# Kernel tuning notes

Measured on AMD Instinct MI355X. Metric: run time of the kernel, lower is better.

The kernel has to match this reference:

```python
import jax, jax.numpy as jnp
import numpy as np

B, S, D, H = 8, 1024, 1024, 16
HD = D // H  # head_dim = 64
MAX_LEN = 1024


def setup_inputs() -> dict:
    key = jax.random.key(0)
    k1, k2, k3, k4, k5 = jax.random.split(key, 5)
    return {
        "query": jax.random.normal(k1, (B, S, D), dtype=jnp.float32),
        "key": jax.random.normal(k2, (B, S, D), dtype=jnp.float32),
        "value": jax.random.normal(k3, (B, S, D), dtype=jnp.float32),
        "rel_pos_k": jax.random.normal(k4, (MAX_LEN, HD), dtype=jnp.float32) * 0.02,
        "rel_pos_v": jax.random.normal(k5, (MAX_LEN, HD), dtype=jnp.float32) * 0.02,
    }


def _circular_indices(seq_len):
    i = jnp.arange(seq_len)
    d = (i[:, None] - i[None, :] + seq_len) % seq_len  # (S, S)
    return jnp.minimum(d, seq_len - d)


def reference(query, key, value, rel_pos_k, rel_pos_v):
    b, s, dm = query.shape
    hd = dm // H
    # (b, h, s, hd)
    q = query.reshape(b, s, H, hd).transpose(0, 2, 1, 3)
    k = key.reshape(b, s, H, hd).transpose(0, 2, 1, 3)
    v = value.reshape(b, s, H, hd).transpose(0, 2, 1, 3)

    scale = 1.0 / np.sqrt(hd)
    scores = jnp.einsum('bhqd,bhkd->bhqk', q, k) * scale

    idx = _circular_indices(s)                 # (s, s) int
    rel_k = rel_pos_k[idx]                     # (s, s, hd)
    rel_v = rel_pos_v[idx]                     # (s, s, hd)

    scores = scores + jnp.einsum('bhqd,qkd->bhqk', q, rel_k)
    attn_weights = jax.nn.softmax(scores, axis=-1)

    out = jnp.einsum('bhqk,bhkd->bhqd', attn_weights, v)
    out = out + jnp.einsum('bhqk,qkd->bhqd', attn_weights, rel_v)

    return out.transpose(0, 2, 1, 3).reshape(b, s, dm)
```

## Files before the change

### kernel.cpp

```cpp
#include <hip/hip_runtime.h>

typedef _Float16 f16;
typedef __attribute__((ext_vector_type(4))) _Float16 f16x4;
typedef __attribute__((ext_vector_type(8))) _Float16 f16x8;
typedef __attribute__((ext_vector_type(4))) float f32x4;
typedef __attribute__((ext_vector_type(4))) unsigned int u32x4;

#define BB 8
#define SS 1024
#define DD 1024
#define HH 16
#define HD 64
#define QPB 32
#define PROW 1040
#define TSTR 520
#define KSTR 72
#define RVSTR 520

#define VT_ELEMS  ((size_t)BB * HH * HD * SS)
#define RVT_ELEMS ((size_t)HD * RVSTR)
#define RKT_ELEMS ((size_t)513 * HD)
#define KT_ELEMS  ((size_t)BB * HH * SS * HD)
#define WS_PART ((VT_ELEMS + RVT_ELEMS + RKT_ELEMS) * 2)
#define WS_FULL ((VT_ELEMS + RVT_ELEMS + RKT_ELEMS + KT_ELEMS) * 2)

__device__ inline f16x8 cvt16(float4 a, float4 b) {
  f16x8 h;
  h[0] = (f16)a.x; h[1] = (f16)a.y; h[2] = (f16)a.z; h[3] = (f16)a.w;
  h[4] = (f16)b.x; h[5] = (f16)b.y; h[6] = (f16)b.z; h[7] = (f16)b.w;
  return h;
}

__device__ inline f16x8 funnel8(u32x4 lo, u32x4 hi, int sh, unsigned lob) {
  unsigned e0 = (sh & 1) ? lo.y : lo.x;
  unsigned e1 = (sh & 1) ? lo.z : lo.y;
  unsigned e2 = (sh & 1) ? lo.w : lo.z;
  unsigned e3 = (sh & 1) ? hi.x : lo.w;
  unsigned e4 = (sh & 1) ? hi.y : hi.x;
  unsigned f0 = (sh & 2) ? e2 : e0;
  unsigned f1 = (sh & 2) ? e3 : e1;
  unsigned f2 = (sh & 2) ? e4 : e2;
  unsigned f3 = (sh & 2) ? ((sh & 1) ? hi.z : hi.y) : e3;
  unsigned f4 = (sh & 2) ? ((sh & 1) ? hi.w : hi.z) : e4;
  union { u32x4 u; f16x8 h; } o;
  o.u.x = __builtin_amdgcn_alignbit(f1, f0, lob);
  o.u.y = __builtin_amdgcn_alignbit(f2, f1, lob);
  o.u.z = __builtin_amdgcn_alignbit(f3, f2, lob);
  o.u.w = __builtin_amdgcn_alignbit(f4, f3, lob);
  return o.h;
}

__device__ inline f16x8 rev8(f16x8 v) {
  union { u32x4 u; f16x8 h; } i, o;
  i.h = v;
  o.u.x = __builtin_amdgcn_alignbit(i.u.w, i.u.w, 16);
  o.u.y = __builtin_amdgcn_alignbit(i.u.z, i.u.z, 16);
  o.u.z = __builtin_amdgcn_alignbit(i.u.y, i.u.y, 16);
  o.u.w = __builtin_amdgcn_alignbit(i.u.x, i.u.x, 16);
  return o.h;
}

__global__ __launch_bounds__(256, 2)
void prep_kernel(const float* __restrict__ Vg, const float* __restrict__ Rvg,
                 const float* __restrict__ Kg, const float* __restrict__ Rkg,
                 f16* __restrict__ Vt, f16* __restrict__ Rvt,
                 f16* __restrict__ Rkt, f16* __restrict__ Kt) {
  __shared__ __align__(16) f16 Tt[64 * KSTR];
  const int tid = threadIdx.x;
  const int bid = blockIdx.x;

  if (bid < 2056) {
    const int sr = tid >> 2, cs = (tid & 3) * 16;
    const float* src;
    int srcstride;
    f16* dst;
    int dststride, dstcol;
    if (bid < 2048) {
      int b = bid >> 8, h = (bid >> 4) & 15, tc = bid & 15;
      src = Vg + ((size_t)(b * SS + tc * 64)) * DD + h * HD;
      srcstride = DD;
      dst = Vt + ((size_t)((b * HH + h) * HD)) * SS;
      dststride = SS; dstcol = tc * 64;
    } else {
      int cc = bid - 2048;
      src = Rvg + ((size_t)(cc * 64)) * HD;
      srcstride = HD;
      dst = Rvt;
      dststride = RVSTR; dstcol = cc * 64;
    }
    {
      const float* s = src + (size_t)sr * srcstride + cs;
      float4 v0 = *(const float4*)(s);
      float4 v1 = *(const float4*)(s + 4);
      float4 v2 = *(const float4*)(s + 8);
      float4 v3 = *(const float4*)(s + 12);
      *(f16x8*)(Tt + sr * KSTR + cs) = cvt16(v0, v1);
      *(f16x8*)(Tt + sr * KSTR + cs + 8) = cvt16(v2, v3);
    }
    __syncthreads();
    {
      f16x8 o0, o1;
      #pragma unroll
      for (int i = 0; i < 8; ++i) o0[i] = Tt[(cs + i) * KSTR + sr];
      #pragma unroll
      for (int i = 0; i < 8; ++i) o1[i] = Tt[(cs + 8 + i) * KSTR + sr];
      f16* o = dst + (size_t)sr * dststride + dstcol + cs;
      *(f16x8*)(o) = o0;
      *(f16x8*)(o + 8) = o1;
    }
  } else if (bid < 2058) {
    const int base = (bid - 2056) * 16416;
    for (int j = tid; j < 16416; j += 256)
      Rkt[base + j] = (f16)Rkg[base + j];
  } else {
    const int n = bid - 2058;
    #pragma unroll
    for (int jj = 0; jj < 4; ++jj) {
      int o4 = n * 1024 + jj * 256 + tid;
      int d4 = o4 & 15;
      int s  = (o4 >> 4) & 1023;
      int bh = o4 >> 14;
      int b = bh >> 4, h = bh & 15;
      float4 v = *(const float4*)(Kg + ((size_t)(b * SS + s)) * DD + h * HD + d4 * 4);
      f16x4 hv; hv[0] = (f16)v.x; hv[1] = (f16)v.y; hv[2] = (f16)v.z; hv[3] = (f16)v.w;
      *(f16x4*)(Kt + (size_t)o4 * 4) = hv;
    }
  }
}

template <bool KT16>
__global__ __launch_bounds__(1024, 4)
void circ_attn_v11(const float* __restrict__ Qg, const float* __restrict__ Kg,
                   const f16* __restrict__ Kt, const f16* __restrict__ Rkt,
                   const float* __restrict__ Rkg, const float* __restrict__ Rvg,
                   const f16* __restrict__ Vt, const f16* __restrict__ Rvt,
                   float* __restrict__ Out) {
  __shared__ __align__(16) f16 Pf[QPB * PROW];
  __shared__ __align__(16) f16 Tb[QPB * TSTR];
  __shared__ __align__(16) f16 Qls[QPB * KSTR];
  __shared__ float lsw[16][32];
  __shared__ float w512[32];

  const int i = blockIdx.x;
  const int g = ((i >> 8) << 3) | (i & 7);
  const int m = (i >> 3) & 31;
  const int b = g >> 4;
  const int h = g & 15;
  const int q0 = m * QPB;

  const int tid = threadIdx.x;
  const int w = tid >> 6;
  const int lane = tid & 63;
  const int quad = lane >> 4;
  const int l16 = lane & 15;
  const int wd = w & 3;
  const int wh = w >> 2;

  if (tid < 256) {
    const int r = tid >> 3;
    const int cg = tid & 7;
    const float* qsrc = Qg + ((size_t)(b * SS + q0 + r)) * DD + h * HD + cg * 8;
    float4 u0 = *(const float4*)(qsrc);
    float4 u1 = *(const float4*)(qsrc + 4);
    *(f16x8*)(Qls + r * KSTR + cg * 8) = cvt16(u0, u1);
  }
  __syncthreads();

  f16x8 qa0, qa1, qb0, qb1;
  {
    const f16* qp = Qls + l16 * KSTR + quad * 8;
    qa0 = *(const f16x8*)(qp);
    qa1 = *(const f16x8*)(qp + 32);
    const f16* qp2 = Qls + (16 + l16) * KSTR + quad * 8;
    qb0 = *(const f16x8*)(qp2);
    qb1 = *(const f16x8*)(qp2 + 32);
  }

  {
    const f16* rkp = Rkt + ((size_t)(w * 16 + l16)) * HD + quad * 8;
    f16x8 t0[2], t1[2];
    #pragma unroll
    for (int t = 0; t < 2; ++t) {
      const f16* np = rkp + (size_t)t * 256 * HD;
      t0[t] = *(const f16x8*)(np);
      t1[t] = *(const f16x8*)(np + 32);
    }
    #pragma unroll
    for (int cc = 0; cc < 2; ++cc) {
      f32x4 ca = {0.f, 0.f, 0.f, 0.f};
      ca = __builtin_amdgcn_mfma_f32_16x16x32_f16(qa0, t0[cc], ca, 0, 0, 0);
      ca = __builtin_amdgcn_mfma_f32_16x16x32_f16(qa1, t1[cc], ca, 0, 0, 0);
      f32x4 cb = {0.f, 0.f, 0.f, 0.f};
      cb = __builtin_amdgcn_mfma_f32_16x16x32_f16(qb0, t0[cc], cb, 0, 0, 0);
      cb = __builtin_amdgcn_mfma_f32_16x16x32_f16(qb1, t1[cc], cb, 0, 0, 0);
      const int dbase = cc * 256 + w * 16 + l16;
      #pragma unroll
      for (int r = 0; r < 4; ++r) {
        Tb[(quad * 4 + r) * TSTR + dbase] = (f16)ca[r];
        Tb[(16 + quad * 4 + r) * TSTR + dbase] = (f16)cb[r];
      }
    }
  }
  if (w == 0) {
    const float* rk = Rkg + 512 * HD;
    float ta = 0.f, tb = 0.f;
    #pragma unroll
    for (int j = 0; j < 8; ++j) {
      float rkv0 = rk[quad * 8 + j], rkv1 = rk[32 + quad * 8 + j];
      ta += (float)qa0[j] * rkv0 + (float)qa1[j] * rkv1;
      tb += (float)qb0[j] * rkv0 + (float)qb1[j] * rkv1;
    }
    ta += __shfl_xor(ta, 16); ta += __shfl_xor(ta, 32);
    tb += __shfl_xor(tb, 16); tb += __shfl_xor(tb, 32);
    if (quad == 0) {
      Tb[l16 * TSTR + 512] = (f16)ta;
      Tb[(16 + l16) * TSTR + 512] = (f16)tb;
    }
  }

  const f16* kp16 = KT16 ?
      (Kt + (((size_t)(b * HH + h) << 10) + w * 16 + l16) * HD + quad * 8) : nullptr;
  const float* kp32 = KT16 ? nullptr :
      (Kg + ((size_t)(b * SS + w * 16 + l16)) * DD + h * HD + quad * 8);
  f16x8 k0[4], k1[4];
  float4 f0, f1, f2, f3;
  if (KT16) {
    #pragma unroll
    for (int t = 0; t < 4; ++t) {
      const f16* np = kp16 + (size_t)t * 256 * HD;
      k0[t] = *(const f16x8*)(np);
      k1[t] = *(const f16x8*)(np + 32);
    }
  } else {
    f0 = *(const float4*)(kp32);
    f1 = *(const float4*)(kp32 + 4);
    f2 = *(const float4*)(kp32 + 32);
    f3 = *(const float4*)(kp32 + 36);
  }
  __syncthreads();

  {
    float psa = 0.f, psb = 0.f;
    #pragma unroll
    for (int kc = 0; kc < 4; ++kc) {
      f16x8 c0, c1;
      if (KT16) {
        c0 = k0[kc]; c1 = k1[kc];
      } else {
        c0 = cvt16(f0, f1); c1 = cvt16(f2, f3);
        if (kc < 3) {
          const float* s = kp32 + (size_t)(kc + 1) * 256 * DD;
          f0 = *(const float4*)(s);      f1 = *(const float4*)(s + 4);
          f2 = *(const float4*)(s + 32); f3 = *(const float4*)(s + 36);
        }
      }
      const int kb_ = kc * 256 + w * 16 + quad * 4;
      const int j0a = ((q0 + l16) - kb_) & 1023;
      const int j0b = (j0a + 16) & 1023;
      float tva[4], tvb[4];
      #pragma unroll
      for (int r = 0; r < 4; ++r) {
        int jra = (j0a - r) & 1023;
        int da = (jra < 1024 - jra) ? jra : 1024 - jra;
        tva[r] = (float)Tb[l16 * TSTR + da];
        int jrb = (j0b - r) & 1023;
        int db = (jrb < 1024 - jrb) ? jrb : 1024 - jrb;
        tvb[r] = (float)Tb[(16 + l16) * TSTR + db];
      }
      f32x4 ca = {0.f, 0.f, 0.f, 0.f};
      ca = __builtin_amdgcn_mfma_f32_16x16x32_f16(c0, qa0, ca, 0, 0, 0);
      ca = __builtin_amdgcn_mfma_f32_16x16x32_f16(c1, qa1, ca, 0, 0, 0);
      f32x4 cb = {0.f, 0.f, 0.f, 0.f};
      cb = __builtin_amdgcn_mfma_f32_16x16x32_f16(c0, qb0, cb, 0, 0, 0);
      cb = __builtin_amdgcn_mfma_f32_16x16x32_f16(c1, qb1, cb, 0, 0, 0);
      f16x4 pva, pvb;
      #pragma unroll
      for (int r = 0; r < 4; ++r) {
        float sa = fmaf(ca[r], 0.125f, tva[r]);
        float pa = __expf(sa);
        pva[r] = (f16)pa; psa += pa;
        float sb = fmaf(cb[r], 0.125f, tvb[r]);
        float pb = __expf(sb);
        pvb[r] = (f16)pb; psb += pb;
      }
      *(f16x4*)(Pf + l16 * PROW + kb_) = pva;
      *(f16x4*)(Pf + (16 + l16) * PROW + kb_) = pvb;
    }
    psa += __shfl_xor(psa, 16); psa += __shfl_xor(psa, 32);
    psb += __shfl_xor(psb, 16); psb += __shfl_xor(psb, 32);
    if (quad == 0) {
      lsw[w][l16] = psa;
      lsw[w][16 + l16] = psb;
    }
  }
  if (w == 0 && lane < 32)
    *(f16x8*)(Pf + lane * PROW + 1024) = *(const f16x8*)(Pf + lane * PROW);

  const f16* vtp = Vt + ((size_t)((b * HH + h) * HD) + wd * 16 + l16) * SS
                      + wh * 256 + quad * 8;
  f16x8 v0[4], v1[4];
  #pragma unroll
  for (int t = 0; t < 4; ++t) {
    v0[t] = *(const f16x8*)(vtp + t * 64);
    v1[t] = *(const f16x8*)(vtp + t * 64 + 32);
  }
  __syncthreads();

  f32x4 coa = {0.f, 0.f, 0.f, 0.f};
  f32x4 cob = {0.f, 0.f, 0.f, 0.f};
  {
    #pragma unroll
    for (int kc = 0; kc < 4; ++kc) {
      const int jb = wh * 256 + kc * 64 + quad * 8;
      f16x8 ap0 = *(const f16x8*)(Pf + l16 * PROW + jb);
      f16x8 ap1 = *(const f16x8*)(Pf + l16 * PROW + jb + 32);
      coa = __builtin_amdgcn_mfma_f32_16x16x32_f16(ap0, v0[kc], coa, 0, 0, 0);
      coa = __builtin_amdgcn_mfma_f32_16x16x32_f16(ap1, v1[kc], coa, 0, 0, 0);
      f16x8 bp0 = *(const f16x8*)(Pf + (16 + l16) * PROW + jb);
      f16x8 bp1 = *(const f16x8*)(Pf + (16 + l16) * PROW + jb + 32);
      cob = __builtin_amdgcn_mfma_f32_16x16x32_f16(bp0, v0[kc], cob, 0, 0, 0);
      cob = __builtin_amdgcn_mfma_f32_16x16x32_f16(bp1, v1[kc], cob, 0, 0, 0);
    }
  }

  const f16* rvp = Rvt + ((size_t)(wd * 16 + l16)) * RVSTR + wh * 128 + quad * 8;
  f16x8 r0[2], r1[2];
  #pragma unroll
  for (int t = 0; t < 2; ++t) {
    r0[t] = *(const f16x8*)(rvp + t * 64);
    r1[t] = *(const f16x8*)(rvp + t * 64 + 32);
  }

  #pragma unroll
  for (int it = 0; it < 2; ++it) {
    const int flat = it * 1024 + tid;
    const int ql = flat >> 6;
    const int gg = flat & 63;
    const int qq = q0 + ql;
    const f16* rowp = Pf + ql * PROW;
    const int sp = qq & 7;
    const int bp = (qq + 8 * gg) & 1023;
    const f16* app = rowp + (bp - sp);
    u32x4 pA = *(const u32x4*)(app);
    u32x4 pB = *(const u32x4*)(app + 8);
    const int sm = (qq + 1) & 7;
    const int bm = (qq - 8 * gg - 7) & 1023;
    const f16* apm = rowp + (bm - sm);
    u32x4 mA = *(const u32x4*)(apm);
    u32x4 mB = *(const u32x4*)(apm + 8);
    f16x8 pp = funnel8(pA, pB, sp >> 1, (unsigned)((sp & 1) * 16));
    f16x8 mw = funnel8(mA, mB, sm >> 1, (unsigned)((sm & 1) * 16));
    f16x8 rm = rev8(mw);
    f16x8 wv = rm + pp;
    if (gg == 0) wv[0] = rm[0];
    *(f16x8*)(Tb + ql * TSTR + gg * 8) = wv;
  }
  if (tid < 32)
    w512[tid] = (float)Pf[tid * PROW + ((q0 + tid + 512) & 1023)];
  __syncthreads();

  {
    #pragma unroll
    for (int cc = 0; cc < 2; ++cc) {
      const int jb = wh * 128 + cc * 64 + quad * 8;
      f16x8 aw0 = *(const f16x8*)(Tb + l16 * TSTR + jb);
      f16x8 aw1 = *(const f16x8*)(Tb + l16 * TSTR + jb + 32);
      coa = __builtin_amdgcn_mfma_f32_16x16x32_f16(aw0, r0[cc], coa, 0, 0, 0);
      coa = __builtin_amdgcn_mfma_f32_16x16x32_f16(aw1, r1[cc], coa, 0, 0, 0);
      f16x8 bw0 = *(const f16x8*)(Tb + (16 + l16) * TSTR + jb);
      f16x8 bw1 = *(const f16x8*)(Tb + (16 + l16) * TSTR + jb + 32);
      cob = __builtin_amdgcn_mfma_f32_16x16x32_f16(bw0, r0[cc], cob, 0, 0, 0);
      cob = __builtin_amdgcn_mfma_f32_16x16x32_f16(bw1, r1[cc], cob, 0, 0, 0);
    }
  }

  if (wh > 0) {
    float* st = (float*)Pf + ((size_t)(((wh - 1) * 4 + wd) * 64 + lane)) * 8;
    *(f32x4*)(st) = coa;
    *(f32x4*)(st + 4) = cob;
  }
  __syncthreads();
  if (wh == 0) {
    #pragma unroll
    for (int p = 0; p < 3; ++p) {
      const float* st = (const float*)Pf + ((size_t)((p * 4 + wd) * 64 + lane)) * 8;
      coa += *(const f32x4*)(st);
      cob += *(const f32x4*)(st + 4);
    }
    const int d = wd * 16 + l16;
    const float rv512 = Rvg[512 * HD + d];
    #pragma unroll
    for (int r = 0; r < 4; ++r) {
      int ql = quad * 4 + r;
      float la = 0.f, lb = 0.f;
      #pragma unroll
      for (int j = 0; j < 16; ++j) { la += lsw[j][ql]; lb += lsw[j][16 + ql]; }
      float oa = coa[r] + w512[ql] * rv512;
      float ob = cob[r] + w512[16 + ql] * rv512;
      Out[((size_t)(b * SS + q0 + ql)) * DD + h * HD + d] = oa / la;
      Out[((size_t)(b * SS + q0 + 16 + ql)) * DD + h * HD + d] = ob / lb;
    }
  }
}

#define FPSTR 1032
#define FVSTR 68
#define FQPB 16
__global__ __launch_bounds__(256, 2)
void circ_attn_mfma(const float* __restrict__ Qg, const float* __restrict__ Kg,
                    const float* __restrict__ Vg, const float* __restrict__ Rkg,
                    const float* __restrict__ Rvg, float* __restrict__ Out) {
  __shared__ __align__(16) f16 Pf[FQPB * FPSTR];
  __shared__ __align__(16) f16 Tb[FQPB * TSTR];
  __shared__ __align__(16) f16 Sb[64 * KSTR];
  __shared__ __align__(16) f16 Qb[FQPB * KSTR];
  __shared__ float lsw[4][16];
  const int bid = blockIdx.x;
  const int b = bid >> 10, h = (bid >> 6) & 15, q0 = (bid & 63) * FQPB;
  const int tid = threadIdx.x, w = tid >> 6, lane = tid & 63;
  const int quad = lane >> 4, l16 = lane & 15;
  auto stage64 = [&](const float* src, int rstride, f16* dst, int dstr) {
    #pragma unroll
    for (int jj = 0; jj < 4; ++jj) {
      int i = jj * 256 + tid;
      int r = i >> 4, c = (i & 15) << 2;
      float4 v = *(const float4*)(src + (size_t)r * rstride + c);
      f16x4 hv; hv[0] = (f16)v.x; hv[1] = (f16)v.y; hv[2] = (f16)v.z; hv[3] = (f16)v.w;
      *(f16x4*)(dst + r * dstr + c) = hv;
    }
  };
  {
    int r = tid >> 4, c = (tid & 15) << 2;
    float4 v = *(const float4*)(Qg + (size_t)(b * SS + q0 + r) * DD + h * HD + c);
    f16x4 hv; hv[0] = (f16)v.x; hv[1] = (f16)v.y; hv[2] = (f16)v.z; hv[3] = (f16)v.w;
    *(f16x4*)(Qb + r * KSTR + c) = hv;
  }
  __syncthreads();
  const f16x8 qf0 = *(const f16x8*)(Qb + l16 * KSTR + quad * 8);
  const f16x8 qf1 = *(const f16x8*)(Qb + l16 * KSTR + 32 + quad * 8);
  #pragma unroll 1
  for (int cc = 0; cc < 8; ++cc) {
    stage64(Rkg + (size_t)(cc * 64) * HD, HD, Sb, KSTR);
    __syncthreads();
    f16x8 rk0 = *(const f16x8*)(Sb + (w * 16 + l16) * KSTR + quad * 8);
    f16x8 rk1 = *(const f16x8*)(Sb + (w * 16 + l16) * KSTR + 32 + quad * 8);
    f32x4 c = {0.f, 0.f, 0.f, 0.f};
    c = __builtin_amdgcn_mfma_f32_16x16x32_f16(qf0, rk0, c, 0, 0, 0);
    c = __builtin_amdgcn_mfma_f32_16x16x32_f16(qf1, rk1, c, 0, 0, 0);
    const int dbase = cc * 64 + w * 16 + l16;
    #pragma unroll
    for (int r = 0; r < 4; ++r) Tb[(quad * 4 + r) * TSTR + dbase] = (f16)c[r];
    __syncthreads();
  }
  if (w == 0) {
    float t = 0.f;
    #pragma unroll
    for (int i = 0; i < 16; ++i)
      t += (float)Qb[l16 * KSTR + quad * 16 + i] * Rkg[512 * HD + quad * 16 + i];
    t += __shfl_xor(t, 16); t += __shfl_xor(t, 32);
    if (quad == 0) Tb[l16 * TSTR + 512] = (f16)t;
  }
  float psum = 0.f;
  #pragma unroll 1
  for (int kc = 0; kc < 16; ++kc) {
    stage64(Kg + (size_t)(b * SS + kc * 64) * DD + h * HD, DD, Sb, KSTR);
    __syncthreads();
    f16x8 ka0 = *(const f16x8*)(Sb + (w * 16 + l16) * KSTR + quad * 8);
    f16x8 ka1 = *(const f16x8*)(Sb + (w * 16 + l16) * KSTR + 32 + quad * 8);
    f32x4 c = {0.f, 0.f, 0.f, 0.f};
    c = __builtin_amdgcn_mfma_f32_16x16x32_f16(ka0, qf0, c, 0, 0, 0);
    c = __builtin_amdgcn_mfma_f32_16x16x32_f16(ka1, qf1, c, 0, 0, 0);
    const int kb = kc * 64 + w * 16 + quad * 4;
    const int q = q0 + l16;
    f16x4 pv;
    #pragma unroll
    for (int r = 0; r < 4; ++r) {
      int key = kb + r;
      int j = (q - key) & 1023;
      int dist = (j < 1024 - j) ? j : 1024 - j;
      float s = c[r] * 0.125f + (float)Tb[l16 * TSTR + dist];
      float p = __expf(s);
      pv[r] = (f16)p;
      psum += p;
    }
    *(f16x4*)(Pf + l16 * FPSTR + kb) = pv;
    __syncthreads();
  }
  psum += __shfl_xor(psum, 16); psum += __shfl_xor(psum, 32);
  if (quad == 0) lsw[w][l16] = psum;
  f32x4 co = {0.f, 0.f, 0.f, 0.f};
  const int d = w * 16 + l16;
  #pragma unroll 1
  for (int kc = 0; kc < 16; ++kc) {
    stage64(Vg + (size_t)(b * SS + kc * 64) * DD + h * HD, DD, Sb, FVSTR);
    __syncthreads();
    #pragma unroll
    for (int kd = 0; kd < 2; ++kd) {
      f16x8 bv;
      #pragma unroll
      for (int j = 0; j < 8; ++j) bv[j] = Sb[(kd * 32 + quad * 8 + j) * FVSTR + d];
      f16x8 ap = *(const f16x8*)(Pf + l16 * FPSTR + kc * 64 + kd * 32 + quad * 8);
      co = __builtin_amdgcn_mfma_f32_16x16x32_f16(ap, bv, co, 0, 0, 0);
    }
    __syncthreads();
  }
  #pragma unroll 1
  for (int i = tid; i < FQPB * 513; i += 256) {
    int ql = i / 513, dist = i - ql * 513, q = q0 + ql;
    int k1 = (q - dist) & 1023;
    float wv = (float)Pf[ql * FPSTR + k1];
    if (dist != 0 && dist != 512) wv += (float)Pf[ql * FPSTR + ((q + dist) & 1023)];
    Tb[ql * TSTR + dist] = (f16)wv;
  }
  __syncthreads();
  #pragma unroll 1
  for (int cc = 0; cc < 8; ++cc) {
    stage64(Rvg + (size_t)(cc * 64) * HD, HD, Sb, FVSTR);
    __syncthreads();
    #pragma unroll
    for (int kd = 0; kd < 2; ++kd) {
      f16x8 bv;
      #pragma unroll
      for (int j = 0; j < 8; ++j) bv[j] = Sb[(kd * 32 + quad * 8 + j) * FVSTR + d];
      f16x8 aw = *(const f16x8*)(Tb + l16 * TSTR + cc * 64 + kd * 32 + quad * 8);
      co = __builtin_amdgcn_mfma_f32_16x16x32_f16(aw, bv, co, 0, 0, 0);
    }
    __syncthreads();
  }
  const float rv512 = Rvg[512 * HD + d];
  #pragma unroll
  for (int r = 0; r < 4; ++r) {
    int ql = quad * 4 + r;
    float l = lsw[0][ql] + lsw[1][ql] + lsw[2][ql] + lsw[3][ql];
    float o = co[r] + (float)Tb[ql * TSTR + 512] * rv512;
    Out[(size_t)(b * SS + q0 + ql) * DD + h * HD + d] = o / l;
  }
}

extern "C" void kernel_launch(void* const* d_in, const int* in_sizes, int n_in,
                              void* d_out, int out_size, void* d_ws, size_t ws_size,
                              hipStream_t stream) {
  const float* q  = (const float*)d_in[0];
  const float* k  = (const float*)d_in[1];
  const float* v  = (const float*)d_in[2];
  const float* rk = (const float*)d_in[3];
  const float* rv = (const float*)d_in[4];
  float* out = (float*)d_out;
  const int nblocks = BB * HH * (SS / QPB);
  f16* vt  = (f16*)d_ws;
  f16* rvt = vt + VT_ELEMS;
  f16* rkt = rvt + RVT_ELEMS;
  f16* kt  = rkt + RKT_ELEMS;
  if (ws_size >= WS_FULL) {
    prep_kernel<<<dim3(2058 + 2048), dim3(256), 0, stream>>>(v, rv, k, rk, vt, rvt, rkt, kt);
    circ_attn_v11<true><<<dim3(nblocks), dim3(1024), 0, stream>>>(
        q, k, kt, rkt, rk, rv, vt, rvt, out);
  } else if (ws_size >= WS_PART) {
    prep_kernel<<<dim3(2058), dim3(256), 0, stream>>>(v, rv, k, rk, vt, rvt, rkt, kt);
    circ_attn_v11<false><<<dim3(nblocks), dim3(1024), 0, stream>>>(
        q, k, kt, rkt, rk, rv, vt, rvt, out);
  } else {
    circ_attn_mfma<<<dim3(8192), dim3(256), 0, stream>>>(q, k, v, rk, rv, out);
  }
}
```

Before: 339.8 us.

## Process two 32-query tiles per block to reuse K and relative-position fragments

Doubles the queries per block to 64 and handles them in two sequential 32-query passes. K, Rk and Rv fragments are loaded into registers once and reused across both passes, which halves the grid and cuts redundant global loads of K per (batch, head). V fragments are now streamed with a two-deep register prefetch instead of all being loaded up front. In exchange, registers stay live across the passes, which adds pressure, and each pass adds more barriers, serialising work inside the block.

```diff
diff --git a/kernel.cpp b/kernel.cpp
--- a/kernel.cpp
+++ b/kernel.cpp
@@ -11,7 +11,7 @@
 #define DD 1024
 #define HH 16
 #define HD 64
-#define QPB 32
+#define QPB 64
 #define PROW 1040
 #define TSTR 520
 #define KSTR 72
@@ -130,20 +130,20 @@
 
 template <bool KT16>
 __global__ __launch_bounds__(1024, 4)
-void circ_attn_v11(const float* __restrict__ Qg, const float* __restrict__ Kg,
+void circ_attn_v12(const float* __restrict__ Qg, const float* __restrict__ Kg,
                    const f16* __restrict__ Kt, const f16* __restrict__ Rkt,
                    const float* __restrict__ Rkg, const float* __restrict__ Rvg,
                    const f16* __restrict__ Vt, const f16* __restrict__ Rvt,
                    float* __restrict__ Out) {
-  __shared__ __align__(16) f16 Pf[QPB * PROW];
-  __shared__ __align__(16) f16 Tb[QPB * TSTR];
+  __shared__ __align__(16) f16 Pf[32 * PROW];
+  __shared__ __align__(16) f16 Tb[32 * TSTR];
   __shared__ __align__(16) f16 Qls[QPB * KSTR];
   __shared__ float lsw[16][32];
   __shared__ float w512[32];
 
   const int i = blockIdx.x;
-  const int g = ((i >> 8) << 3) | (i & 7);
-  const int m = (i >> 3) & 31;
+  const int g = ((i >> 7) << 3) | (i & 7);
+  const int m = (i >> 3) & 15;
   const int b = g >> 4;
   const int h = g & 15;
   const int q0 = m * QPB;
@@ -156,7 +156,7 @@
   const int wd = w & 3;
   const int wh = w >> 2;
 
-  if (tid < 256) {
+  if (tid < 512) {
     const int r = tid >> 3;
     const int cg = tid & 7;
     const float* qsrc = Qg + ((size_t)(b * SS + q0 + r)) * DD + h * HD + cg * 8;
@@ -164,27 +164,53 @@
     float4 u1 = *(const float4*)(qsrc + 4);
     *(f16x8*)(Qls + r * KSTR + cg * 8) = cvt16(u0, u1);
   }
+
+  const f16* rkp = Rkt + ((size_t)(w * 16 + l16)) * HD + quad * 8;
+  f16x8 t0[2], t1[2];
+  #pragma unroll
+  for (int t = 0; t < 2; ++t) {
+    const f16* np = rkp + (size_t)t * 256 * HD;
+    t0[t] = *(const f16x8*)(np);
+    t1[t] = *(const f16x8*)(np + 32);
+  }
+  const f16* kp16 = KT16 ?
+      (Kt + (((size_t)(b * HH + h) << 10) + w * 16 + l16) * HD + quad * 8) : nullptr;
+  const float* kp32 = KT16 ? nullptr :
+      (Kg + ((size_t)(b * SS + w * 16 + l16)) * DD + h * HD + quad * 8);
+  f16x8 k0[4], k1[4];
+  if (KT16) {
+    #pragma unroll
+    for (int t = 0; t < 4; ++t) {
+      const f16* np = kp16 + (size_t)t * 256 * HD;
+      k0[t] = *(const f16x8*)(np);
+      k1[t] = *(const f16x8*)(np + 32);
+    }
+  }
+  const f16* rvp = Rvt + ((size_t)(wd * 16 + l16)) * RVSTR + wh * 128 + quad * 8;
+  f16x8 r0[2], r1[2];
+  #pragma unroll
+  for (int t = 0; t < 2; ++t) {
+    r0[t] = *(const f16x8*)(rvp + t * 64);
+    r1[t] = *(const f16x8*)(rvp + t * 64 + 32);
+  }
+  const f16* vtp = Vt + ((size_t)((b * HH + h) * HD) + wd * 16 + l16) * SS
+                      + wh * 256 + quad * 8;
   __syncthreads();
 
-  f16x8 qa0, qa1, qb0, qb1;
-  {
-    const f16* qp = Qls + l16 * KSTR + quad * 8;
-    qa0 = *(const f16x8*)(qp);
-    qa1 = *(const f16x8*)(qp + 32);
-    const f16* qp2 = Qls + (16 + l16) * KSTR + quad * 8;
-    qb0 = *(const f16x8*)(qp2);
-    qb1 = *(const f16x8*)(qp2 + 32);
-  }
-
-  {
-    const f16* rkp = Rkt + ((size_t)(w * 16 + l16)) * HD + quad * 8;
-    f16x8 t0[2], t1[2];
-    #pragma unroll
-    for (int t = 0; t < 2; ++t) {
-      const f16* np = rkp + (size_t)t * 256 * HD;
-      t0[t] = *(const f16x8*)(np);
-      t1[t] = *(const f16x8*)(np + 32);
-    }
+  #pragma unroll
+  for (int tt = 0; tt < 2; ++tt) {
+    const int qb = q0 + tt * 32;
+
+    f16x8 qa0, qa1, qb0, qb1;
+    {
+      const f16* qp = Qls + (tt * 32 + l16) * KSTR + quad * 8;
+      qa0 = *(const f16x8*)(qp);
+      qa1 = *(const f16x8*)(qp + 32);
+      const f16* qp2 = Qls + (tt * 32 + 16 + l16) * KSTR + quad * 8;
+      qb0 = *(const f16x8*)(qp2);
+      qb1 = *(const f16x8*)(qp2 + 32);
+    }
+
     #pragma unroll
     for (int cc = 0; cc < 2; ++cc) {
       f32x4 ca = {0.f, 0.f, 0.f, 0.f};
@@ -200,166 +226,144 @@
         Tb[(16 + quad * 4 + r) * TSTR + dbase] = (f16)cb[r];
       }
     }
-  }
-  if (w == 0) {
-    const float* rk = Rkg + 512 * HD;
-    float ta = 0.f, tb = 0.f;
-    #pragma unroll
-    for (int j = 0; j < 8; ++j) {
-      float rkv0 = rk[quad * 8 + j], rkv1 = rk[32 + quad * 8 + j];
-      ta += (float)qa0[j] * rkv0 + (float)qa1[j] * rkv1;
-      tb += (float)qb0[j] * rkv0 + (float)qb1[j] * rkv1;
-    }
-    ta += __shfl_xor(ta, 16); ta += __shfl_xor(ta, 32);
-    tb += __shfl_xor(tb, 16); tb += __shfl_xor(tb, 32);
-    if (quad == 0) {
-      Tb[l16 * TSTR + 512] = (f16)ta;
-      Tb[(16 + l16) * TSTR + 512] = (f16)tb;
-    }
-  }
-
-  const f16* kp16 = KT16 ?
-      (Kt + (((size_t)(b * HH + h) << 10) + w * 16 + l16) * HD + quad * 8) : nullptr;
-  const float* kp32 = KT16 ? nullptr :
-      (Kg + ((size_t)(b * SS + w * 16 + l16)) * DD + h * HD + quad * 8);
-  f16x8 k0[4], k1[4];
-  float4 f0, f1, f2, f3;
-  if (KT16) {
-    #pragma unroll
-    for (int t = 0; t < 4; ++t) {
-      const f16* np = kp16 + (size_t)t * 256 * HD;
-      k0[t] = *(const f16x8*)(np);
-      k1[t] = *(const f16x8*)(np + 32);
-    }
-  } else {
-    f0 = *(const float4*)(kp32);
-    f1 = *(const float4*)(kp32 + 4);
-    f2 = *(const float4*)(kp32 + 32);
-    f3 = *(const float4*)(kp32 + 36);
-  }
-  __syncthreads();
-
-  {
-    float psa = 0.f, psb = 0.f;
+    if (w == 0) {
+      const float* rk = Rkg + 512 * HD;
+      float ta = 0.f, tb2 = 0.f;
+      #pragma unroll
+      for (int j = 0; j < 8; ++j) {
+        float rkv0 = rk[quad * 8 + j], rkv1 = rk[32 + quad * 8 + j];
+        ta  += (float)qa0[j] * rkv0 + (float)qa1[j] * rkv1;
+        tb2 += (float)qb0[j] * rkv0 + (float)qb1[j] * rkv1;
+      }
+      ta += __shfl_xor(ta, 16); ta += __shfl_xor(ta, 32);
+      tb2 += __shfl_xor(tb2, 16); tb2 += __shfl_xor(tb2, 32);
+      if (quad == 0) {
+        Tb[l16 * TSTR + 512] = (f16)ta;
+        Tb[(16 + l16) * TSTR + 512] = (f16)tb2;
+      }
+    }
+
+    float4 f0, f1, f2, f3;
+    if (!KT16) {
+      f0 = *(const float4*)(kp32);
+      f1 = *(const float4*)(kp32 + 4);
+      f2 = *(const float4*)(kp32 + 32);
+      f3 = *(const float4*)(kp32 + 36);
+    }
+    __syncthreads();
+
+    {
+      float psa = 0.f, psb = 0.f;
+      #pragma unroll
+      for (int kc = 0; kc < 4; ++kc) {
+        f16x8 c0, c1;
+        if (KT16) {
+          c0 = k0[kc]; c1 = k1[kc];
+        } else {
+          c0 = cvt16(f0, f1); c1 = cvt16(f2, f3);
+          if (kc < 3) {
+            const float* s = kp32 + (size_t)(kc + 1) * 256 * DD;
+            f0 = *(const float4*)(s);      f1 = *(const float4*)(s + 4);
+            f2 = *(const float4*)(s + 32); f3 = *(const float4*)(s + 36);
+          }
+        }
+        const int kb_ = kc * 256 + w * 16 + quad * 4;
+        const int j0a = ((qb + l16) - kb_) & 1023;
+        const int j0b = (j0a + 16) & 1023;
+        float tva[4], tvb[4];
+        #pragma unroll
+        for (int r = 0; r < 4; ++r) {
+          int jra = (j0a - r) & 1023;
+          int da = (jra < 1024 - jra) ? jra : 1024 - jra;
+          tva[r] = (float)Tb[l16 * TSTR + da];
+          int jrb = (j0b - r) & 1023;
+          int db = (jrb < 1024 - jrb) ? jrb : 1024 - jrb;
+          tvb[r] = (float)Tb[(16 + l16) * TSTR + db];
+        }
+        f32x4 ca = {0.f, 0.f, 0.f, 0.f};
+        ca = __builtin_amdgcn_mfma_f32_16x16x32_f16(c0, qa0, ca, 0, 0, 0);
+        ca = __builtin_amdgcn_mfma_f32_16x16x32_f16(c1, qa1, ca, 0, 0, 0);
+        f32x4 cb = {0.f, 0.f, 0.f, 0.f};
+        cb = __builtin_amdgcn_mfma_f32_16x16x32_f16(c0, qb0, cb, 0, 0, 0);
+        cb = __builtin_amdgcn_mfma_f32_16x16x32_f16(c1, qb1, cb, 0, 0, 0);
+        f16x4 pva, pvb;
+        #pragma unroll
+        for (int r = 0; r < 4; ++r) {
+          float sa = fmaf(ca[r], 0.125f, tva[r]);
+          float pa = __expf(sa);
+          pva[r] = (f16)pa; psa += pa;
+          float sb = fmaf(cb[r], 0.125f, tvb[r]);
+          float pb = __expf(sb);
+          pvb[r] = (f16)pb; psb += pb;
+        }
+        *(f16x4*)(Pf + l16 * PROW + kb_) = pva;
+        *(f16x4*)(Pf + (16 + l16) * PROW + kb_) = pvb;
+      }
+      psa += __shfl_xor(psa, 16); psa += __shfl_xor(psa, 32);
+      psb += __shfl_xor(psb, 16); psb += __shfl_xor(psb, 32);
+      if (quad == 0) {
+        lsw[w][l16] = psa;
+        lsw[w][16 + l16] = psb;
+      }
+    }
+    if (w == 0 && lane < 32)
+      *(f16x8*)(Pf + lane * PROW + 1024) = *(const f16x8*)(Pf + lane * PROW);
+
+    f16x8 va0 = *(const f16x8*)(vtp);
+    f16x8 va1 = *(const f16x8*)(vtp + 32);
+    f16x8 vb0 = *(const f16x8*)(vtp + 64);
+    f16x8 vb1 = *(const f16x8*)(vtp + 96);
+    __syncthreads();
+
+    f32x4 coa = {0.f, 0.f, 0.f, 0.f};
+    f32x4 cob = {0.f, 0.f, 0.f, 0.f};
     #pragma unroll
     for (int kc = 0; kc < 4; ++kc) {
-      f16x8 c0, c1;
-      if (KT16) {
-        c0 = k0[kc]; c1 = k1[kc];
-      } else {
-        c0 = cvt16(f0, f1); c1 = cvt16(f2, f3);
-        if (kc < 3) {
-          const float* s = kp32 + (size_t)(kc + 1) * 256 * DD;
-          f0 = *(const float4*)(s);      f1 = *(const float4*)(s + 4);
-          f2 = *(const float4*)(s + 32); f3 = *(const float4*)(s + 36);
-        }
-      }
-      const int kb_ = kc * 256 + w * 16 + quad * 4;
-      const int j0a = ((q0 + l16) - kb_) & 1023;
-      const int j0b = (j0a + 16) & 1023;
-      float tva[4], tvb[4];
-      #pragma unroll
-      for (int r = 0; r < 4; ++r) {
-        int jra = (j0a - r) & 1023;
-        int da = (jra < 1024 - jra) ? jra : 1024 - jra;
-        tva[r] = (float)Tb[l16 * TSTR + da];
-        int jrb = (j0b - r) & 1023;
-        int db = (jrb < 1024 - jrb) ? jrb : 1024 - jrb;
-        tvb[r] = (float)Tb[(16 + l16) * TSTR + db];
-      }
-      f32x4 ca = {0.f, 0.f, 0.f, 0.f};
-      ca = __builtin_amdgcn_mfma_f32_16x16x32_f16(c0, qa0, ca, 0, 0, 0);
-      ca = __builtin_amdgcn_mfma_f32_16x16x32_f16(c1, qa1, ca, 0, 0, 0);
-      f32x4 cb = {0.f, 0.f, 0.f, 0.f};
-      cb = __builtin_amdgcn_mfma_f32_16x16x32_f16(c0, qb0, cb, 0, 0, 0);
-      cb = __builtin_amdgcn_mfma_f32_16x16x32_f16(c1, qb1, cb, 0, 0, 0);
-      f16x4 pva, pvb;
-      #pragma unroll
-      for (int r = 0; r < 4; ++r) {
-        float sa = fmaf(ca[r], 0.125f, tva[r]);
-        float pa = __expf(sa);
-        pva[r] = (f16)pa; psa += pa;
-        float sb = fmaf(cb[r], 0.125f, tvb[r]);
-        float pb = __expf(sb);
-        pvb[r] = (f16)pb; psb += pb;
-      }
-      *(f16x4*)(Pf + l16 * PROW + kb_) = pva;
-      *(f16x4*)(Pf + (16 + l16) * PROW + kb_) = pvb;
-    }
-    psa += __shfl_xor(psa, 16); psa += __shfl_xor(psa, 32);
-    psb += __shfl_xor(psb, 16); psb += __shfl_xor(psb, 32);
-    if (quad == 0) {
-      lsw[w][l16] = psa;
-      lsw[w][16 + l16] = psb;
-    }
-  }
-  if (w == 0 && lane < 32)
-    *(f16x8*)(Pf + lane * PROW + 1024) = *(const f16x8*)(Pf + lane * PROW);
-
-  const f16* vtp = Vt + ((size_t)((b * HH + h) * HD) + wd * 16 + l16) * SS
-                      + wh * 256 + quad * 8;
-  f16x8 v0[4], v1[4];
-  #pragma unroll
-  for (int t = 0; t < 4; ++t) {
-    v0[t] = *(const f16x8*)(vtp + t * 64);
-    v1[t] = *(const f16x8*)(vtp + t * 64 + 32);
-  }
-  __syncthreads();
-
-  f32x4 coa = {0.f, 0.f, 0.f, 0.f};
-  f32x4 cob = {0.f, 0.f, 0.f, 0.f};
-  {
-    #pragma unroll
-    for (int kc = 0; kc < 4; ++kc) {
+      f16x8 cv0 = va0, cv1 = va1;
+      va0 = vb0; va1 = vb1;
+      if (kc < 2) {
+        vb0 = *(const f16x8*)(vtp + (kc + 2) * 64);
+        vb1 = *(const f16x8*)(vtp + (kc + 2) * 64 + 32);
+      }
       const int jb = wh * 256 + kc * 64 + quad * 8;
       f16x8 ap0 = *(const f16x8*)(Pf + l16 * PROW + jb);
       f16x8 ap1 = *(const f16x8*)(Pf + l16 * PROW + jb + 32);
-      coa = __builtin_amdgcn_mfma_f32_16x16x32_f16(ap0, v0[kc], coa, 0, 0, 0);
-      coa = __builtin_amdgcn_mfma_f32_16x16x32_f16(ap1, v1[kc], coa, 0, 0, 0);
+      coa = __builtin_amdgcn_mfma_f32_16x16x32_f16(ap0, cv0, coa, 0, 0, 0);
+      coa = __builtin_amdgcn_mfma_f32_16x16x32_f16(ap1, cv1, coa, 0, 0, 0);
       f16x8 bp0 = *(const f16x8*)(Pf + (16 + l16) * PROW + jb);
       f16x8 bp1 = *(const f16x8*)(Pf + (16 + l16) * PROW + jb + 32);
-      cob = __builtin_amdgcn_mfma_f32_16x16x32_f16(bp0, v0[kc], cob, 0, 0, 0);
-      cob = __builtin_amdgcn_mfma_f32_16x16x32_f16(bp1, v1[kc], cob, 0, 0, 0);
-    }
-  }
-
-  const f16* rvp = Rvt + ((size_t)(wd * 16 + l16)) * RVSTR + wh * 128 + quad * 8;
-  f16x8 r0[2], r1[2];
-  #pragma unroll
-  for (int t = 0; t < 2; ++t) {
-    r0[t] = *(const f16x8*)(rvp + t * 64);
-    r1[t] = *(const f16x8*)(rvp + t * 64 + 32);
-  }
-
-  #pragma unroll
-  for (int it = 0; it < 2; ++it) {
-    const int flat = it * 1024 + tid;
-    const int ql = flat >> 6;
-    const int gg = flat & 63;
-    const int qq = q0 + ql;
-    const f16* rowp = Pf + ql * PROW;
-    const int sp = qq & 7;
-    const int bp = (qq + 8 * gg) & 1023;
-    const f16* app = rowp + (bp - sp);
-    u32x4 pA = *(const u32x4*)(app);
-    u32x4 pB = *(const u32x4*)(app + 8);
-    const int sm = (qq + 1) & 7;
-    const int bm = (qq - 8 * gg - 7) & 1023;
-    const f16* apm = rowp + (bm - sm);
-    u32x4 mA = *(const u32x4*)(apm);
-    u32x4 mB = *(const u32x4*)(apm + 8);
-    f16x8 pp = funnel8(pA, pB, sp >> 1, (unsigned)((sp & 1) * 16));
-    f16x8 mw = funnel8(mA, mB, sm >> 1, (unsigned)((sm & 1) * 16));
-    f16x8 rm = rev8(mw);
-    f16x8 wv = rm + pp;
-    if (gg == 0) wv[0] = rm[0];
-    *(f16x8*)(Tb + ql * TSTR + gg * 8) = wv;
-  }
-  if (tid < 32)
-    w512[tid] = (float)Pf[tid * PROW + ((q0 + tid + 512) & 1023)];
-  __syncthreads();
-
-  {
+      cob = __builtin_amdgcn_mfma_f32_16x16x32_f16(bp0, cv0, cob, 0, 0, 0);
+      cob = __builtin_amdgcn_mfma_f32_16x16x32_f16(bp1, cv1, cob, 0, 0, 0);
+    }
+
+    #pragma unroll
+    for (int it = 0; it < 2; ++it) {
+      const int flat = it * 1024 + tid;
+      const int ql = flat >> 6;
+      const int gg = flat & 63;
+      const int qq = qb + ql;
+      const f16* rowp = Pf + ql * PROW;
+      const int sp = qq & 7;
+      const int bp = (qq + 8 * gg) & 1023;
+      const f16* app = rowp + (bp - sp);
+      u32x4 pA = *(const u32x4*)(app);
+      u32x4 pB = *(const u32x4*)(app + 8);
+      const int sm = (qq + 1) & 7;
+      const int bm = (qq - 8 * gg - 7) & 1023;
+      const f16* apm = rowp + (bm - sm);
+      u32x4 mA = *(const u32x4*)(apm);
+      u32x4 mB = *(const u32x4*)(apm + 8);
+      f16x8 pp = funnel8(pA, pB, sp >> 1, (unsigned)((sp & 1) * 16));
+      f16x8 mw = funnel8(mA, mB, sm >> 1, (unsigned)((sm & 1) * 16));
+      f16x8 rm = rev8(mw);
+      f16x8 wv = rm + pp;
+      if (gg == 0) wv[0] = rm[0];
+      *(f16x8*)(Tb + ql * TSTR + gg * 8) = wv;
+    }
+    if (tid < 32)
+      w512[tid] = (float)Pf[tid * PROW + ((qb + tid + 512) & 1023)];
+    __syncthreads();
+
     #pragma unroll
     for (int cc = 0; cc < 2; ++cc) {
       const int jb = wh * 128 + cc * 64 + quad * 8;
@@ -372,33 +376,33 @@
       cob = __builtin_amdgcn_mfma_f32_16x16x32_f16(bw0, r0[cc], cob, 0, 0, 0);
       cob = __builtin_amdgcn_mfma_f32_16x16x32_f16(bw1, r1[cc], cob, 0, 0, 0);
     }
-  }
-
-  if (wh > 0) {
-    float* st = (float*)Pf + ((size_t)(((wh - 1) * 4 + wd) * 64 + lane)) * 8;
-    *(f32x4*)(st) = coa;
-    *(f32x4*)(st + 4) = cob;
-  }
-  __syncthreads();
-  if (wh == 0) {
-    #pragma unroll
-    for (int p = 0; p < 3; ++p) {
-      const float* st = (const float*)Pf + ((size_t)((p * 4 + wd) * 64 + lane)) * 8;
-      coa += *(const f32x4*)(st);
-      cob += *(const f32x4*)(st + 4);
-    }
-    const int d = wd * 16 + l16;
-    const float rv512 = Rvg[512 * HD + d];
-    #pragma unroll
-    for (int r = 0; r < 4; ++r) {
-      int ql = quad * 4 + r;
-      float la = 0.f, lb = 0.f;
-      #pragma unroll
-      for (int j = 0; j < 16; ++j) { la += lsw[j][ql]; lb += lsw[j][16 + ql]; }
-      float oa = coa[r] + w512[ql] * rv512;
-      float ob = cob[r] + w512[16 + ql] * rv512;
-      Out[((size_t)(b * SS + q0 + ql)) * DD + h * HD + d] = oa / la;
-      Out[((size_t)(b * SS + q0 + 16 + ql)) * DD + h * HD + d] = ob / lb;
+
+    if (wh > 0) {
+      float* st = (float*)Pf + ((size_t)(((wh - 1) * 4 + wd) * 64 + lane)) * 8;
+      *(f32x4*)(st) = coa;
+      *(f32x4*)(st + 4) = cob;
+    }
+    __syncthreads();
+    if (wh == 0) {
+      #pragma unroll
+      for (int p = 0; p < 3; ++p) {
+        const float* st = (const float*)Pf + ((size_t)((p * 4 + wd) * 64 + lane)) * 8;
+        coa += *(const f32x4*)(st);
+        cob += *(const f32x4*)(st + 4);
+      }
+      const int d = wd * 16 + l16;
+      const float rv512 = Rvg[512 * HD + d];
+      #pragma unroll
+      for (int r = 0; r < 4; ++r) {
+        int ql = quad * 4 + r;
+        float la = 0.f, lb = 0.f;
+        #pragma unroll
+        for (int j = 0; j < 16; ++j) { la += lsw[j][ql]; lb += lsw[j][16 + ql]; }
+        float oa = coa[r] + w512[ql] * rv512;
+        float ob = cob[r] + w512[16 + ql] * rv512;
+        Out[((size_t)(b * SS + qb + ql)) * DD + h * HD + d] = oa / la;
+        Out[((size_t)(b * SS + qb + 16 + ql)) * DD + h * HD + d] = ob / lb;
+      }
     }
   }
 }
@@ -553,11 +557,11 @@
   f16* kt  = rkt + RKT_ELEMS;
   if (ws_size >= WS_FULL) {
     prep_kernel<<<dim3(2058 + 2048), dim3(256), 0, stream>>>(v, rv, k, rk, vt, rvt, rkt, kt);
-    circ_attn_v11<true><<<dim3(nblocks), dim3(1024), 0, stream>>>(
+    circ_attn_v12<true><<<dim3(nblocks), dim3(1024), 0, stream>>>(
         q, k, kt, rkt, rk, rv, vt, rvt, out);
   } else if (ws_size >= WS_PART) {
     prep_kernel<<<dim3(2058), dim3(256), 0, stream>>>(v, rv, k, rk, vt, rvt, rkt, kt);
-    circ_attn_v11<false><<<dim3(nblocks), dim3(1024), 0, stream>>>(
+    circ_attn_v12<false><<<dim3(nblocks), dim3(1024), 0, stream>>>(
         q, k, kt, rkt, rk, rv, vt, rvt, out);
   } else {
     circ_attn_mfma<<<dim3(8192), dim3(256), 0, stream>>>(q, k, v, rk, rv, out);
```

Measured after the change: 418.0 us. +23.0%, slower.
